# Performance work log

Hardware: AMD Instinct MI355X
Metric: run time of the kernel (lower is better)

The kernel has to match this reference:

```python
import jax, jax.numpy as jnp
import numpy as np
from jax import lax


def setup_inputs() -> dict:
    key = jax.random.key(0)
    ks = jax.random.split(key, 6)
    B = 65536
    x = jax.random.normal(ks[0], (B, 784), dtype=jnp.float32)
    conv_w = jax.random.normal(ks[1], (3, 3), dtype=jnp.float32)
    w1 = jax.random.normal(ks[2], (676, 128), dtype=jnp.float32) * 0.05
    b1 = jax.random.normal(ks[3], (128,), dtype=jnp.float32) * 0.05
    w2 = jax.random.normal(ks[4], (128, 10), dtype=jnp.float32) * 0.05
    b2 = jax.random.normal(ks[5], (10,), dtype=jnp.float32) * 0.05
    return {"x": x, "conv_w": conv_w, "w1": w1, "b1": b1, "w2": w2, "b2": b2}


def reference(x, conv_w, w1, b1, w2, b2):
    B = x.shape[0]
    img = x.reshape(B, 1, 28, 28)  # NCHW
    # valid 3x3 cross-correlation (tensordot over patch == cross-correlation)
    conv = lax.conv_general_dilated(
        img, conv_w[None, None], window_strides=(1, 1), padding="VALID",
        dimension_numbers=("NCHW", "OIHW", "NCHW"))  # [B,1,26,26]
    h = conv.reshape(B, 26 * 26)
    h = jax.nn.relu(h @ w1 + b1)
    return h @ w2 + b2
```

## Files before the change

kernel.cpp:

```cpp
#include <hip/hip_runtime.h>

typedef __attribute__((ext_vector_type(4))) float floatx4;
typedef __attribute__((ext_vector_type(8))) short short8;
typedef __attribute__((ext_vector_type(4))) unsigned short ushort4v;
typedef __attribute__((ext_vector_type(8))) unsigned short ushort8v;

__device__ __forceinline__ unsigned short f2bf(float f) {
  unsigned int u = __builtin_bit_cast(unsigned int, f);
  u += 0x7FFFu + ((u >> 16) & 1u);
  return (unsigned short)(u >> 16);
}

#define KTOT 784
#define KP   800
#define N1   128
#define BM   128
#define BK   32
#define LDA  40
#define LDH  136

__global__ void prep_w1eff(const float* __restrict__ conv_w,
                           const float* __restrict__ w1,
                           unsigned short* __restrict__ Bt) {
  const int n = blockIdx.x;
  float cw[9];
#pragma unroll
  for (int i = 0; i < 9; ++i) cw[i] = conv_w[i];
  for (int q = threadIdx.x; q < KP; q += blockDim.x) {
    float acc = 0.f;
    if (q < KTOT) {
      const int r = q / 28, c = q % 28;
#pragma unroll
      for (int di = 0; di < 3; ++di) {
        const int i2 = r - di;
        if (i2 < 0 || i2 >= 26) continue;
#pragma unroll
        for (int dj = 0; dj < 3; ++dj) {
          const int j2 = c - dj;
          if (j2 < 0 || j2 >= 26) continue;
          acc += cw[di * 3 + dj] * w1[(i2 * 26 + j2) * N1 + n];
        }
      }
    }
    Bt[n * KP + q] = f2bf(acc);
  }
}

__global__ __launch_bounds__(256, 2)
void fused_mlp(const float* __restrict__ x,
               const unsigned short* __restrict__ Bt,
               const float* __restrict__ b1,
               const float* __restrict__ w2,
               const float* __restrict__ b2,
               float* __restrict__ out) {
  __shared__ __align__(16) unsigned short sA[BM * LDA];
  __shared__ __align__(16) unsigned short sB[N1 * LDA];
  __shared__ __align__(16) unsigned short sH[BM * LDH];
  __shared__ __align__(16) unsigned short sW2t[16 * LDH];
  __shared__ float sB1[N1];
  __shared__ float sB2[16];

  const int tid  = threadIdx.x;
  const int wave = tid >> 6;
  const int lane = tid & 63;
  const int wm = wave & 1;
  const int wn = wave >> 1;
  const int lr = lane & 15;
  const int lq = lane >> 4;

  const long row_base = (long)blockIdx.x * BM;
  const float* xblk = x + row_base * KTOT;

  for (int i = tid; i < 16 * N1; i += 256) {
    const int n = i >> 7, k = i & 127;
    sW2t[n * LDH + k] = (n < 10) ? f2bf(w2[k * 10 + n]) : (unsigned short)0;
  }
  if (tid < N1) sB1[tid] = b1[tid];
  if (tid < 10) sB2[tid] = b2[tid];

  const int akp = tid & 7;
  const int arp = tid >> 3;
  const int bkp = tid & 3;
  const int bnp = tid >> 2;

  floatx4 acc[4][4] = {};

  for (int kt = 0; kt < 25; ++kt) {
    const int k0 = kt * BK;
    __syncthreads();
#pragma unroll
    for (int p = 0; p < 4; ++p) {
      const int row = p * 32 + arp;
      const int kk = k0 + akp * 4;
      floatx4 v = {0.f, 0.f, 0.f, 0.f};
      if (kk < KTOT) v = *(const floatx4*)(xblk + row * KTOT + kk);
      ushort4v u;
      u[0] = f2bf(v[0]); u[1] = f2bf(v[1]); u[2] = f2bf(v[2]); u[3] = f2bf(v[3]);
      *(ushort4v*)&sA[row * LDA + akp * 4] = u;
    }
#pragma unroll
    for (int p = 0; p < 2; ++p) {
      const int n = p * 64 + bnp;
      const ushort8v g = *(const ushort8v*)(Bt + n * KP + k0 + bkp * 8);
      *(ushort8v*)&sB[n * LDA + bkp * 8] = g;
    }
    __syncthreads();
    short8 af[4], bfv[4];
#pragma unroll
    for (int i = 0; i < 4; ++i)
      af[i] = *(const short8*)&sA[(wm * 64 + i * 16 + lr) * LDA + lq * 8];
#pragma unroll
    for (int i = 0; i < 4; ++i)
      bfv[i] = *(const short8*)&sB[(wn * 64 + i * 16 + lr) * LDA + lq * 8];
#pragma unroll
    for (int im = 0; im < 4; ++im)
#pragma unroll
      for (int in = 0; in < 4; ++in)
        acc[im][in] = __builtin_amdgcn_mfma_f32_16x16x32_bf16(
            af[im], bfv[in], acc[im][in], 0, 0, 0);
  }

#pragma unroll
  for (int im = 0; im < 4; ++im) {
#pragma unroll
    for (int in = 0; in < 4; ++in) {
      const int col = wn * 64 + in * 16 + lr;
      const float bb = sB1[col];
#pragma unroll
      for (int r = 0; r < 4; ++r) {
        const int row = wm * 64 + im * 16 + lq * 4 + r;
        const float v = acc[im][in][r] + bb;
        sH[row * LDH + col] = f2bf(v > 0.f ? v : 0.f);
      }
    }
  }
  __syncthreads();

  floatx4 o0 = {0.f, 0.f, 0.f, 0.f}, o1 = {0.f, 0.f, 0.f, 0.f};
  const int m0 = wave * 32;
#pragma unroll
  for (int kc = 0; kc < 4; ++kc) {
    const int kof = kc * 32 + lq * 8;
    const short8 wv = *(const short8*)&sW2t[lr * LDH + kof];
    const short8 a0 = *(const short8*)&sH[(m0 + lr) * LDH + kof];
    const short8 a1 = *(const short8*)&sH[(m0 + 16 + lr) * LDH + kof];
    o0 = __builtin_amdgcn_mfma_f32_16x16x32_bf16(a0, wv, o0, 0, 0, 0);
    o1 = __builtin_amdgcn_mfma_f32_16x16x32_bf16(a1, wv, o1, 0, 0, 0);
  }
  if (lr < 10) {
    const float bb = sB2[lr];
#pragma unroll
    for (int r = 0; r < 4; ++r) {
      const long row = row_base + m0 + lq * 4 + r;
      out[row * 10 + lr] = o0[r] + bb;
      out[(row + 16) * 10 + lr] = o1[r] + bb;
    }
  }
}

extern "C" void kernel_launch(void* const* d_in, const int* in_sizes, int n_in,
                              void* d_out, int out_size, void* d_ws, size_t ws_size,
                              hipStream_t stream) {
  const float* x      = (const float*)d_in[0];
  const float* conv_w = (const float*)d_in[1];
  const float* w1     = (const float*)d_in[2];
  const float* b1     = (const float*)d_in[3];
  const float* w2     = (const float*)d_in[4];
  const float* b2     = (const float*)d_in[5];
  float* out = (float*)d_out;

  unsigned short* Bt = (unsigned short*)d_ws;

  prep_w1eff<<<128, 256, 0, stream>>>(conv_w, w1, Bt);
  fused_mlp<<<65536 / BM, 256, 0, stream>>>(x, Bt, b1, w2, b2, out);
}
```

Before: 323.0 us.

## Double-buffer LDS tiles with register prefetch and LDS-only barriers

Restructures the K loop into a software pipeline. The next x and Bt tiles are loaded into registers while the current tile is in LDS, and LDS holds two ping-pong buffers. The barriers now wait only on LDS counters, so global loads can stay in flight across the MFMA step. This hides HBM latency in what should be a bandwidth-bound kernel. The LDS row padding also shrinks, which may give 128-bit LDS reads that are not 16-byte aligned, and the out-of-range K tail is clamped instead of zeroed, which relies on the zero padding in Bt.

```diff
diff --git a/kernel.cpp b/kernel.cpp
--- a/kernel.cpp
+++ b/kernel.cpp
@@ -16,8 +16,10 @@
 #define N1   128
 #define BM   128
 #define BK   32
-#define LDA  40
-#define LDH  136
+#define LDA  36
+#define LDH  132
+
+#define LBAR() do { __builtin_amdgcn_s_waitcnt(0xC07F); __builtin_amdgcn_s_barrier(); } while (0)
 
 __global__ void prep_w1eff(const float* __restrict__ conv_w,
                            const float* __restrict__ w1,
@@ -53,8 +55,8 @@
                const float* __restrict__ w2,
                const float* __restrict__ b2,
                float* __restrict__ out) {
-  __shared__ __align__(16) unsigned short sA[BM * LDA];
-  __shared__ __align__(16) unsigned short sB[N1 * LDA];
+  __shared__ __align__(16) unsigned short sA[2 * BM * LDA];
+  __shared__ __align__(16) unsigned short sB[2 * N1 * LDA];
   __shared__ __align__(16) unsigned short sH[BM * LDH];
   __shared__ __align__(16) unsigned short sW2t[16 * LDH];
   __shared__ float sB1[N1];
@@ -85,40 +87,75 @@
 
   floatx4 acc[4][4] = {};
 
-  for (int kt = 0; kt < 25; ++kt) {
+  auto load_a = [&](floatx4* pa, int kt) {
     const int k0 = kt * BK;
-    __syncthreads();
 #pragma unroll
     for (int p = 0; p < 4; ++p) {
       const int row = p * 32 + arp;
-      const int kk = k0 + akp * 4;
-      floatx4 v = {0.f, 0.f, 0.f, 0.f};
-      if (kk < KTOT) v = *(const floatx4*)(xblk + row * KTOT + kk);
-      ushort4v u;
-      u[0] = f2bf(v[0]); u[1] = f2bf(v[1]); u[2] = f2bf(v[2]); u[3] = f2bf(v[3]);
-      *(ushort4v*)&sA[row * LDA + akp * 4] = u;
-    }
+      int kk = k0 + akp * 4;
+      if (kk >= KTOT) kk = KTOT - 16;
+      pa[p] = *(const floatx4*)(xblk + (long)row * KTOT + kk);
+    }
+  };
+  auto load_b = [&](ushort8v* pb, int kt) {
+    const int k0 = kt * BK;
 #pragma unroll
     for (int p = 0; p < 2; ++p) {
       const int n = p * 64 + bnp;
-      const ushort8v g = *(const ushort8v*)(Bt + n * KP + k0 + bkp * 8);
-      *(ushort8v*)&sB[n * LDA + bkp * 8] = g;
-    }
-    __syncthreads();
+      pb[p] = *(const ushort8v*)(Bt + n * KP + k0 + bkp * 8);
+    }
+  };
+  auto store_tile = [&](int buf, const floatx4* pa, const ushort8v* pb) {
+    unsigned short* A  = sA + buf * (BM * LDA);
+    unsigned short* Bs = sB + buf * (N1 * LDA);
+#pragma unroll
+    for (int p = 0; p < 4; ++p) {
+      ushort4v u;
+      u[0] = f2bf(pa[p][0]); u[1] = f2bf(pa[p][1]);
+      u[2] = f2bf(pa[p][2]); u[3] = f2bf(pa[p][3]);
+      *(ushort4v*)&A[(p * 32 + arp) * LDA + akp * 4] = u;
+    }
+#pragma unroll
+    for (int p = 0; p < 2; ++p)
+      *(ushort8v*)&Bs[(p * 64 + bnp) * LDA + bkp * 8] = pb[p];
+  };
+  auto mfma_step = [&](int buf) {
+    const unsigned short* A  = sA + buf * (BM * LDA);
+    const unsigned short* Bs = sB + buf * (N1 * LDA);
     short8 af[4], bfv[4];
 #pragma unroll
     for (int i = 0; i < 4; ++i)
-      af[i] = *(const short8*)&sA[(wm * 64 + i * 16 + lr) * LDA + lq * 8];
+      af[i] = *(const short8*)&A[(wm * 64 + i * 16 + lr) * LDA + lq * 8];
 #pragma unroll
     for (int i = 0; i < 4; ++i)
-      bfv[i] = *(const short8*)&sB[(wn * 64 + i * 16 + lr) * LDA + lq * 8];
+      bfv[i] = *(const short8*)&Bs[(wn * 64 + i * 16 + lr) * LDA + lq * 8];
 #pragma unroll
     for (int im = 0; im < 4; ++im)
 #pragma unroll
       for (int in = 0; in < 4; ++in)
         acc[im][in] = __builtin_amdgcn_mfma_f32_16x16x32_bf16(
             af[im], bfv[in], acc[im][in], 0, 0, 0);
-  }
+  };
+
+  floatx4 pa0[4], pa1[4];
+  ushort8v pb0[2], pb1[2];
+  load_a(pa0, 0);
+  load_b(pb0, 0);
+  for (int kt = 0; kt < 24; kt += 2) {
+    load_a(pa1, kt + 1);
+    load_b(pb1, kt + 1);
+    store_tile(0, pa0, pb0);
+    LBAR();
+    mfma_step(0);
+    load_a(pa0, kt + 2);
+    load_b(pb0, kt + 2);
+    store_tile(1, pa1, pb1);
+    LBAR();
+    mfma_step(1);
+  }
+  store_tile(0, pa0, pb0);
+  LBAR();
+  mfma_step(0);
 
 #pragma unroll
   for (int im = 0; im < 4; ++im) {
```

Result: faster. 306.6 us (-5.1%).

## Load MFMA fragments directly from global into double-buffered registers, drop LDS staging

Applied to the files above, without the earlier changes.

Removes the shared-memory staging of the x and weight tiles and the two barriers per K-step. Each lane now loads its MFMA fragments straight from global memory into registers, converts x to bf16 in registers, and prefetches the next K-tile while computing the current one. The last K-tile reuses an in-bounds offset so the loads stay inside the row, relying on the zero-padded weights to cancel those terms. The trade-offs are extra register pressure, duplicate x reads across the two N-waves, and less coalesced strided row loads. The hidden-activation LDS row pitch also shrinks, which changes bank mapping and 16-byte alignment of the vector reads.

```diff
diff --git a/kernel.cpp b/kernel.cpp
--- a/kernel.cpp
+++ b/kernel.cpp
@@ -2,7 +2,6 @@
 
 typedef __attribute__((ext_vector_type(4))) float floatx4;
 typedef __attribute__((ext_vector_type(8))) short short8;
-typedef __attribute__((ext_vector_type(4))) unsigned short ushort4v;
 typedef __attribute__((ext_vector_type(8))) unsigned short ushort8v;
 
 __device__ __forceinline__ unsigned short f2bf(float f) {
@@ -16,8 +15,7 @@
 #define N1   128
 #define BM   128
 #define BK   32
-#define LDA  40
-#define LDH  136
+#define LDH  132
 
 __global__ void prep_w1eff(const float* __restrict__ conv_w,
                            const float* __restrict__ w1,
@@ -53,8 +51,6 @@
                const float* __restrict__ w2,
                const float* __restrict__ b2,
                float* __restrict__ out) {
-  __shared__ __align__(16) unsigned short sA[BM * LDA];
-  __shared__ __align__(16) unsigned short sB[N1 * LDA];
   __shared__ __align__(16) unsigned short sH[BM * LDH];
   __shared__ __align__(16) unsigned short sW2t[16 * LDH];
   __shared__ float sB1[N1];
@@ -69,7 +65,6 @@
   const int lq = lane >> 4;
 
   const long row_base = (long)blockIdx.x * BM;
-  const float* xblk = x + row_base * KTOT;
 
   for (int i = tid; i < 16 * N1; i += 256) {
     const int n = i >> 7, k = i & 127;
@@ -78,47 +73,67 @@
   if (tid < N1) sB1[tid] = b1[tid];
   if (tid < 10) sB2[tid] = b2[tid];
 
-  const int akp = tid & 7;
-  const int arp = tid >> 3;
-  const int bkp = tid & 3;
-  const int bnp = tid >> 2;
+  const float* aptr[4];
+  const unsigned short* bptr[4];
+#pragma unroll
+  for (int i = 0; i < 4; ++i) {
+    aptr[i] = x + (row_base + wm * 64 + i * 16 + lr) * (long)KTOT + lq * 8;
+    bptr[i] = Bt + (wn * 64 + i * 16 + lr) * KP + lq * 8;
+  }
 
   floatx4 acc[4][4] = {};
 
-  for (int kt = 0; kt < 25; ++kt) {
+  auto load_a = [&](floatx4* pa, int kt) {
+    int k0 = kt * BK;
+    if (kt == 24 && lq >= 2) k0 = 736;
+#pragma unroll
+    for (int i = 0; i < 4; ++i) {
+      pa[2 * i]     = *(const floatx4*)(aptr[i] + k0);
+      pa[2 * i + 1] = *(const floatx4*)(aptr[i] + k0 + 4);
+    }
+  };
+  auto load_b = [&](ushort8v* pb, int kt) {
     const int k0 = kt * BK;
-    __syncthreads();
 #pragma unroll
-    for (int p = 0; p < 4; ++p) {
-      const int row = p * 32 + arp;
-      const int kk = k0 + akp * 4;
-      floatx4 v = {0.f, 0.f, 0.f, 0.f};
-      if (kk < KTOT) v = *(const floatx4*)(xblk + row * KTOT + kk);
-      ushort4v u;
-      u[0] = f2bf(v[0]); u[1] = f2bf(v[1]); u[2] = f2bf(v[2]); u[3] = f2bf(v[3]);
-      *(ushort4v*)&sA[row * LDA + akp * 4] = u;
-    }
-#pragma unroll
-    for (int p = 0; p < 2; ++p) {
-      const int n = p * 64 + bnp;
-      const ushort8v g = *(const ushort8v*)(Bt + n * KP + k0 + bkp * 8);
-      *(ushort8v*)&sB[n * LDA + bkp * 8] = g;
-    }
-    __syncthreads();
+    for (int i = 0; i < 4; ++i)
+      pb[i] = *(const ushort8v*)(bptr[i] + k0);
+  };
+  auto compute = [&](const floatx4* pa, const ushort8v* pb) {
     short8 af[4], bfv[4];
 #pragma unroll
-    for (int i = 0; i < 4; ++i)
-      af[i] = *(const short8*)&sA[(wm * 64 + i * 16 + lr) * LDA + lq * 8];
+    for (int i = 0; i < 4; ++i) {
+      ushort8v u;
 #pragma unroll
-    for (int i = 0; i < 4; ++i)
-      bfv[i] = *(const short8*)&sB[(wn * 64 + i * 16 + lr) * LDA + lq * 8];
+      for (int j = 0; j < 4; ++j) {
+        u[j]     = f2bf(pa[2 * i][j]);
+        u[4 + j] = f2bf(pa[2 * i + 1][j]);
+      }
+      af[i]  = __builtin_bit_cast(short8, u);
+      bfv[i] = __builtin_bit_cast(short8, pb[i]);
+    }
 #pragma unroll
     for (int im = 0; im < 4; ++im)
 #pragma unroll
       for (int in = 0; in < 4; ++in)
         acc[im][in] = __builtin_amdgcn_mfma_f32_16x16x32_bf16(
             af[im], bfv[in], acc[im][in], 0, 0, 0);
+  };
+
+  floatx4 pa0[8], pa1[8];
+  ushort8v pb0[4], pb1[4];
+  load_a(pa0, 0);
+  load_b(pb0, 0);
+  for (int kt = 0; kt < 24; kt += 2) {
+    load_a(pa1, kt + 1);
+    load_b(pb1, kt + 1);
+    compute(pa0, pb0);
+    load_a(pa0, kt + 2);
+    load_b(pb0, kt + 2);
+    compute(pa1, pb1);
   }
+  compute(pa0, pb0);
+
+  __syncthreads();
 
 #pragma unroll
   for (int im = 0; im < 4; ++im) {
```

After: 336.4 us. 4.1% more time.

## Double-buffer x tiles via global_load_lds DMA and read W1 fragments from global

Applied to the files above, without the earlier changes.

The main loop now streams fp32 x tiles straight into a swizzled, double-buffered LDS region with global_load_lds, so the next tile is prefetched while the current one feeds MFMA. The bf16 conversion moves to after the LDS read. W1 fragments are loaded directly from global/L2 into registers instead of being staged through LDS. The block grows to 512 threads (8 waves) with smaller per-wave tiles, and the hidden-activation buffer aliases the A buffer to cut LDS use. The goal is to hide HBM latency and drop one barrier per K step, at the cost of hand-written waitcnt ordering and a trick for the tail tile.

```diff
diff --git a/kernel.cpp b/kernel.cpp
--- a/kernel.cpp
+++ b/kernel.cpp
@@ -2,7 +2,6 @@
 
 typedef __attribute__((ext_vector_type(4))) float floatx4;
 typedef __attribute__((ext_vector_type(8))) short short8;
-typedef __attribute__((ext_vector_type(4))) unsigned short ushort4v;
 typedef __attribute__((ext_vector_type(8))) unsigned short ushort8v;
 
 __device__ __forceinline__ unsigned short f2bf(float f) {
@@ -15,9 +14,13 @@
 #define KP   800
 #define N1   128
 #define BM   128
-#define BK   32
-#define LDA  40
-#define LDH  136
+#define LDH  132
+
+typedef const __attribute__((address_space(1))) unsigned int* gas_ptr;
+typedef __attribute__((address_space(3))) unsigned int* las_ptr;
+__device__ __forceinline__ void dma16(const float* g, float* l) {
+  __builtin_amdgcn_global_load_lds((gas_ptr)g, (las_ptr)l, 16, 0, 0);
+}
 
 __global__ void prep_w1eff(const float* __restrict__ conv_w,
                            const float* __restrict__ w1,
@@ -46,89 +49,104 @@
   }
 }
 
-__global__ __launch_bounds__(256, 2)
+__global__ __launch_bounds__(512, 4)
 void fused_mlp(const float* __restrict__ x,
                const unsigned short* __restrict__ Bt,
                const float* __restrict__ b1,
                const float* __restrict__ w2,
                const float* __restrict__ b2,
                float* __restrict__ out) {
-  __shared__ __align__(16) unsigned short sA[BM * LDA];
-  __shared__ __align__(16) unsigned short sB[N1 * LDA];
-  __shared__ __align__(16) unsigned short sH[BM * LDH];
-  __shared__ __align__(16) unsigned short sW2t[16 * LDH];
-  __shared__ float sB1[N1];
-  __shared__ float sB2[16];
+  __shared__ __align__(16) unsigned char smem[38592];
+  float* sAf = (float*)smem;
+  unsigned short* sH = (unsigned short*)smem;
+  unsigned short* sW2t = (unsigned short*)(smem + 33792);
+  float* sB1 = (float*)(smem + 38016);
+  float* sB2 = (float*)(smem + 38528);
 
   const int tid  = threadIdx.x;
   const int wave = tid >> 6;
   const int lane = tid & 63;
-  const int wm = wave & 1;
-  const int wn = wave >> 1;
+  const int wm = wave >> 1;
+  const int wn = wave & 1;
   const int lr = lane & 15;
   const int lq = lane >> 4;
 
   const long row_base = (long)blockIdx.x * BM;
   const float* xblk = x + row_base * KTOT;
 
-  for (int i = tid; i < 16 * N1; i += 256) {
+  for (int i = tid; i < 16 * N1; i += 512) {
     const int n = i >> 7, k = i & 127;
     sW2t[n * LDH + k] = (n < 10) ? f2bf(w2[k * 10 + n]) : (unsigned short)0;
   }
   if (tid < N1) sB1[tid] = b1[tid];
-  if (tid < 10) sB2[tid] = b2[tid];
+  if (tid >= N1 && tid < N1 + 10) sB2[tid - N1] = b2[tid - N1];
 
-  const int akp = tid & 7;
-  const int arp = tid >> 3;
-  const int bkp = tid & 3;
-  const int bnp = tid >> 2;
+  const int i0 = wave * 2, i1 = wave * 2 + 1;
+  const int rsub = lane >> 3;
+  const int cg = (lane & 7) ^ (rsub & 6);
+  const int ceff = (cg < 4) ? cg : cg - 4;
+  const float* gA0 = xblk + (long)(i0 * 8 + rsub) * KTOT + cg * 4;
+  const float* gA1 = xblk + (long)(i1 * 8 + rsub) * KTOT + cg * 4;
+  const float* gT0 = xblk + (long)(i0 * 8 + rsub) * KTOT + 768 + ceff * 4;
+  const float* gT1 = xblk + (long)(i1 * 8 + rsub) * KTOT + 768 + ceff * 4;
 
-  floatx4 acc[4][4] = {};
+  const unsigned short* bptr[4];
+#pragma unroll
+  for (int in = 0; in < 4; ++in)
+    bptr[in] = Bt + (long)(wn * 64 + in * 16 + lr) * KP + lq * 8;
+
+  floatx4 acc[2][4] = {};
+
+  dma16(gA0, sAf + i0 * 256);
+  dma16(gA1, sAf + i1 * 256);
 
   for (int kt = 0; kt < 25; ++kt) {
-    const int k0 = kt * BK;
-    __syncthreads();
+    const int buf = kt & 1;
+    ushort8v rB[4];
 #pragma unroll
-    for (int p = 0; p < 4; ++p) {
-      const int row = p * 32 + arp;
-      const int kk = k0 + akp * 4;
-      floatx4 v = {0.f, 0.f, 0.f, 0.f};
-      if (kk < KTOT) v = *(const floatx4*)(xblk + row * KTOT + kk);
-      ushort4v u;
-      u[0] = f2bf(v[0]); u[1] = f2bf(v[1]); u[2] = f2bf(v[2]); u[3] = f2bf(v[3]);
-      *(ushort4v*)&sA[row * LDA + akp * 4] = u;
+    for (int in = 0; in < 4; ++in)
+      rB[in] = *(const ushort8v*)(bptr[in] + kt * 32);
+    asm volatile("s_waitcnt vmcnt(4)\n\ts_barrier" ::: "memory");
+    {
+      const int d = (kt + 1 <= 24) ? kt + 1 : 24;
+      const float* g0 = (d < 24) ? gA0 + d * 32 : gT0;
+      const float* g1 = (d < 24) ? gA1 + d * 32 : gT1;
+      float* ldst = sAf + (buf ^ 1) * 4096;
+      dma16(g0, ldst + i0 * 256);
+      dma16(g1, ldst + i1 * 256);
+    }
+    const float* A = sAf + buf * 4096;
+    short8 af[2];
+#pragma unroll
+    for (int im = 0; im < 2; ++im) {
+      const int r = wm * 32 + im * 16 + lr;
+      const int s0 = (2 * lq) ^ (r & 6);
+      const floatx4* p = (const floatx4*)(A + r * 32 + s0 * 4);
+      const floatx4 q0 = p[0], q1 = p[1];
+      ushort8v u;
+#pragma unroll
+      for (int j = 0; j < 4; ++j) { u[j] = f2bf(q0[j]); u[4 + j] = f2bf(q1[j]); }
+      af[im] = __builtin_bit_cast(short8, u);
     }
 #pragma unroll
-    for (int p = 0; p < 2; ++p) {
-      const int n = p * 64 + bnp;
-      const ushort8v g = *(const ushort8v*)(Bt + n * KP + k0 + bkp * 8);
-      *(ushort8v*)&sB[n * LDA + bkp * 8] = g;
-    }
-    __syncthreads();
-    short8 af[4], bfv[4];
-#pragma unroll
-    for (int i = 0; i < 4; ++i)
-      af[i] = *(const short8*)&sA[(wm * 64 + i * 16 + lr) * LDA + lq * 8];
-#pragma unroll
-    for (int i = 0; i < 4; ++i)
-      bfv[i] = *(const short8*)&sB[(wn * 64 + i * 16 + lr) * LDA + lq * 8];
-#pragma unroll
-    for (int im = 0; im < 4; ++im)
+    for (int im = 0; im < 2; ++im)
 #pragma unroll
       for (int in = 0; in < 4; ++in)
         acc[im][in] = __builtin_amdgcn_mfma_f32_16x16x32_bf16(
-            af[im], bfv[in], acc[im][in], 0, 0, 0);
+            af[im], __builtin_bit_cast(short8, rB[in]), acc[im][in], 0, 0, 0);
   }
 
+  __syncthreads();
+
 #pragma unroll
-  for (int im = 0; im < 4; ++im) {
+  for (int im = 0; im < 2; ++im) {
 #pragma unroll
     for (int in = 0; in < 4; ++in) {
       const int col = wn * 64 + in * 16 + lr;
       const float bb = sB1[col];
 #pragma unroll
       for (int r = 0; r < 4; ++r) {
-        const int row = wm * 64 + im * 16 + lq * 4 + r;
+        const int row = wm * 32 + im * 16 + lq * 4 + r;
         const float v = acc[im][in][r] + bb;
         sH[row * LDH + col] = f2bf(v > 0.f ? v : 0.f);
       }
@@ -136,24 +154,21 @@
   }
   __syncthreads();
 
-  floatx4 o0 = {0.f, 0.f, 0.f, 0.f}, o1 = {0.f, 0.f, 0.f, 0.f};
-  const int m0 = wave * 32;
+  floatx4 o = {0.f, 0.f, 0.f, 0.f};
+  const int m0 = wave * 16;
 #pragma unroll
   for (int kc = 0; kc < 4; ++kc) {
     const int kof = kc * 32 + lq * 8;
     const short8 wv = *(const short8*)&sW2t[lr * LDH + kof];
     const short8 a0 = *(const short8*)&sH[(m0 + lr) * LDH + kof];
-    const short8 a1 = *(const short8*)&sH[(m0 + 16 + lr) * LDH + kof];
-    o0 = __builtin_amdgcn_mfma_f32_16x16x32_bf16(a0, wv, o0, 0, 0, 0);
-    o1 = __builtin_amdgcn_mfma_f32_16x16x32_bf16(a1, wv, o1, 0, 0, 0);
+    o = __builtin_amdgcn_mfma_f32_16x16x32_bf16(a0, wv, o, 0, 0, 0);
   }
   if (lr < 10) {
     const float bb = sB2[lr];
 #pragma unroll
     for (int r = 0; r < 4; ++r) {
       const long row = row_base + m0 + lq * 4 + r;
-      out[row * 10 + lr] = o0[r] + bb;
-      out[(row + 16) * 10 + lr] = o1[r] + bb;
+      out[row * 10 + lr] = o[r] + bb;
     }
   }
 }
@@ -172,5 +187,5 @@
   unsigned short* Bt = (unsigned short*)d_ws;
 
   prep_w1eff<<<128, 256, 0, stream>>>(conv_w, w1, Bt);
-  fused_mlp<<<65536 / BM, 256, 0, stream>>>(x, Bt, b1, w2, b2, out);
+  fused_mlp<<<65536 / BM, 512, 0, stream>>>(x, Bt, b1, w2, b2, out);
 }
```

After: 306.9 us. 1.05x faster.
